# Performance work log

Measured on AMD Instinct MI355X. Metric: run time of the kernel, lower is better.

Reference implementation:

```python
import jax, jax.numpy as jnp
import numpy as np

NMS_THR = 0.5
SCORE_THR = 0.05
MAX_BOXES = 300
N_ANCHORS = 5000
N_CLASSES = 80
IMG = 640.0  # image size used to scale synthetic box coords


def setup_inputs() -> dict:
    key = jax.random.key(0)
    k1, k2, k3 = jax.random.split(key, 3)
    # build well-formed boxes (x1<=x2, y1<=y2) in a 640x640 image
    c1 = jax.random.uniform(k1, (1, N_ANCHORS, 2), jnp.float32) * IMG
    c2 = jax.random.uniform(k2, (1, N_ANCHORS, 2), jnp.float32) * IMG
    boxes = jnp.concatenate([jnp.minimum(c1, c2), jnp.maximum(c1, c2) + 1.0], axis=-1)
    # classification scores in [0,1], squared to skew toward low values like sigmoid logits
    classification = jax.random.uniform(k3, (1, N_ANCHORS, N_CLASSES), jnp.float32) ** 2
    return {"boxes": boxes, "classification": classification}


def _iou_matrix(b):
    # b: [N,4] as (x1,y1,x2,y2) -> [N,N] pairwise IoU
    x1, y1, x2, y2 = b[:, 0], b[:, 1], b[:, 2], b[:, 3]
    area = (x2 - x1) * (y2 - y1)
    iw = jnp.maximum(jnp.minimum(x2[:, None], x2[None, :]) - jnp.maximum(x1[:, None], x1[None, :]), 0.0)
    ih = jnp.maximum(jnp.minimum(y2[:, None], y2[None, :]) - jnp.maximum(y1[:, None], y1[None, :]), 0.0)
    inter = iw * ih
    union = area[:, None] + area[None, :] - inter
    return inter / jnp.maximum(union, 1e-8)


def _nms_one_class(scores, iou):
    # greedy NMS for one class; scores: [N], iou: [N,N] (shared across classes)
    n = scores.shape[0]
    order = jnp.argsort(-scores)          # descending score order
    valid = scores > SCORE_THR            # per-class score-threshold filter
    idxs = jnp.arange(n)

    def step(carry, oi):
        suppressed, kept, count = carry
        alive = (~suppressed[oi]) & valid[oi] & (count < MAX_BOXES)
        # a kept box suppresses all others with IoU above threshold
        suppressed = suppressed | (alive & (iou[oi] > NMS_THR) & (idxs != oi))
        kept = kept.at[oi].set(alive)
        return (suppressed, kept, count + alive.astype(jnp.int32)), None

    init = (jnp.zeros(n, jnp.bool_), jnp.zeros(n, jnp.bool_), jnp.int32(0))
    (_, kept, _), _ = jax.lax.scan(step, init, order)
    return kept  # [N] bool mask in original index space


def reference(boxes, classification):
    b = boxes[0]             # [N,4]
    cls = classification[0]  # [N,C]
    iou = _iou_matrix(b)     # [N,N], class-independent
    kept = jax.vmap(_nms_one_class, in_axes=(1, None))(cls, iou)  # [C,N]
    # scatter surviving scores back to dense per-class score map (zeros elsewhere)
    selected = jnp.where(kept.T, cls, 0.0)                        # [N,C]
    detections = jnp.concatenate([b, selected], axis=1)           # [N,4+C]
    return detections[None]                                       # [1,N,4+C]
```

## Files before the change

### kernel.cpp

```cpp
#include <hip/hip_runtime.h>

#define N_ANCHORS 5000
#define N_CLASSES 80
#define OUT_COLS  84
#define MAX_BOXES 300
#define SCORE_THR 0.05f

#define SORT_PAD  5056
#define NB        4096
#define BLOCK     1024
#define IR        16
#define KR        16
#define DONEP     0x40000000

typedef unsigned long long u64;
typedef unsigned int u32;

#define WG __HIP_MEMORY_SCOPE_WORKGROUP

__device__ __forceinline__ float readlane_f(float v, int l) {
    return __int_as_float(__builtin_amdgcn_readlane(__float_as_int(v), l));
}
__device__ __forceinline__ u32 aload(u32* p) {
    return __hip_atomic_load(p, __ATOMIC_ACQUIRE, WG);
}
__device__ __forceinline__ int bucket_of(float s) {
    float u = sqrtf(s);
    int b = (int)((u - 0.2236f) * 5275.0f);
    return min(max(b, 0), NB - 1);
}
__device__ __forceinline__ bool iou_gt(float4 a, float aa, float4 b, float ab) {
    float iw = fmaxf(fminf(a.z, b.z) - fmaxf(a.x, b.x), 0.0f);
    float ih = fmaxf(fminf(a.w, b.w) - fmaxf(a.y, b.y), 0.0f);
    return 3.0f * (iw * ih) > aa + ab;
}

#define INIT_BLKS 1641
#define TR_BX     157
#define TR_BY     3
#define TR_BLKS   (TR_BX * TR_BY)

__global__ __launch_bounds__(256) void prep(const float* __restrict__ boxes,
                                            const float* __restrict__ cls,
                                            float* __restrict__ clsT,
                                            float* __restrict__ out) {
    __shared__ float tile[32][33];
    int b = blockIdx.x;
    if (b < INIT_BLKS) {
        int i = b * 256 + threadIdx.x;
        if (i < N_ANCHORS * OUT_COLS) {
            int row = i / OUT_COLS, col = i - row * OUT_COLS;
            out[i] = (col < 4) ? boxes[row * 4 + col] : 0.0f;
        }
        return;
    }
    b -= INIT_BLKS;
    int bx_ = b % TR_BX, by_ = b / TR_BX;
    int j0 = bx_ * 32, c0 = by_ * 32;
    int tx = threadIdx.x & 31, ty = threadIdx.x >> 5;
    #pragma unroll
    for (int r = 0; r < 32; r += 8) {
        int j = j0 + ty + r, c = c0 + tx;
        tile[ty + r][tx] = (j < N_ANCHORS && c < N_CLASSES) ? cls[j * N_CLASSES + c] : 0.0f;
    }
    __syncthreads();
    #pragma unroll
    for (int r = 0; r < 32; r += 8) {
        int c = c0 + ty + r, j = j0 + tx;
        if (c < N_CLASSES && j < N_ANCHORS) clsT[(size_t)c * N_ANCHORS + j] = tile[tx][ty + r];
    }
}

__global__ __launch_bounds__(BLOCK, 1) void nms(const float* __restrict__ clsT,
                                                const float4* __restrict__ boxes4,
                                                float* __restrict__ out) {
    __shared__ u64 lk[SORT_PAD];
    __shared__ u32 hist[NB];
    __shared__ float4 kbox[MAX_BOXES + 4];
    __shared__ u64 KS[KR];
    __shared__ u32 flagI[IR], flagK[KR], KBa[KR];
    __shared__ u32 wtot[16];
    __shared__ u32 prog, kcnt;
    u64* Iring = (u64*)hist;

    const int c = blockIdx.x;
    const int t = threadIdx.x;
    const int lane = t & 63;
    const int wv = t >> 6;

    const float4* cp4 = (const float4*)(clsT + (size_t)c * N_ANCHORS);
    u32 sb[8];
    #pragma unroll
    for (int m = 0; m < 2; ++m) {
        int vi = m * 1024 + t;
        float4 v = make_float4(0.f, 0.f, 0.f, 0.f);
        if (vi < N_ANCHORS / 4) v = cp4[vi];
        sb[m * 4 + 0] = (v.x > SCORE_THR) ? __float_as_uint(v.x) : 0u;
        sb[m * 4 + 1] = (v.y > SCORE_THR) ? __float_as_uint(v.y) : 0u;
        sb[m * 4 + 2] = (v.z > SCORE_THR) ? __float_as_uint(v.z) : 0u;
        sb[m * 4 + 3] = (v.w > SCORE_THR) ? __float_as_uint(v.w) : 0u;
    }
    for (int b = t; b < NB; b += BLOCK) hist[b] = 0u;
    if (t < IR) { flagI[t] = 0u; flagK[t] = 0u; }
    if (t == 0) { prog = 0u; kcnt = 0u; }
    __syncthreads();
    #pragma unroll
    for (int m = 0; m < 8; ++m)
        if (sb[m]) atomicAdd(&hist[bucket_of(__uint_as_float(sb[m]))], 1u);
    __syncthreads();

    const int hbase = t * 4;
    u32 vals[4]; u32 run = 0;
    #pragma unroll
    for (int k = 0; k < 4; ++k) { run += hist[hbase + k]; vals[k] = run; }
    u32 x = run;
    #pragma unroll
    for (int off = 1; off < 64; off <<= 1) { u32 y = __shfl_up(x, off); if (lane >= off) x += y; }
    if (lane == 63) wtot[wv] = x;
    __syncthreads();
    u32 woff = 0;
    for (int w = 0; w < wv; ++w) woff += wtot[w];
    const u32 exb = woff + x - run;
    #pragma unroll
    for (int k = 0; k < 4; ++k) hist[hbase + k] = exb + (k ? vals[k - 1] : 0u);
    __syncthreads();
    #pragma unroll
    for (int m = 0; m < 8; ++m) {
        if (sb[m]) {
            int j = ((m >> 2) * 1024 + t) * 4 + (m & 3);
            u32 pos = atomicAdd(&hist[bucket_of(__uint_as_float(sb[m]))], 1u);
            lk[pos] = ((u64)sb[m] << 32) | (u32)(~(u32)j);
        }
    }
    __syncthreads();
    const int total = (int)hist[NB - 1];
    for (int v = total + t; v < SORT_PAD; v += BLOCK) lk[v] = 0ull;
    for (int b = hbase; b < hbase + 4; ++b) {
        int s0 = b ? (int)hist[b - 1] : 0;
        int e  = (int)hist[b];
        for (int i = s0 + 1; i < e; ++i) {
            u64 key = lk[i]; int q = i - 1;
            while (q >= s0 && lk[q] < key) { lk[q + 1] = lk[q]; --q; }
            lk[q + 1] = key;
        }
    }
    __syncthreads();
    const int nch = (total + 63) >> 6;

    if (wv >= 1 && wv <= 8) {
        for (int j = wv - 1; j < nch; j += 8) {
            u32 p;
            for (;;) {
                p = aload(&prog);
                if ((int)p >= j - (IR - 1)) break;
                __builtin_amdgcn_s_sleep(2);
            }
            if (p >= DONEP) return;
            u64 e = lk[j * 64 + lane];
            u32 jj = e ? ~(u32)e : 0u;
            float4 bx = boxes4[jj];
            float ar = (bx.z - bx.x) * (bx.w - bx.y);
            u64 word = 0ull;
            #pragma unroll 16
            for (int q = 0; q < 64; ++q) {
                float4 o;
                o.x = readlane_f(bx.x, q); o.y = readlane_f(bx.y, q);
                o.z = readlane_f(bx.z, q); o.w = readlane_f(bx.w, q);
                float ao = (o.z - o.x) * (o.w - o.y);
                if (iou_gt(bx, ar, o, ao)) word |= (1ull << q);
            }
            Iring[(j & (IR - 1)) * 64 + lane] = word;
            if (lane == 0)
                __hip_atomic_store(&flagI[j & (IR - 1)], (u32)(j + 1), __ATOMIC_RELEASE, WG);
        }
        return;
    }
    if (wv >= 9) {
        for (int j = wv - 9; j < nch; j += 7) {
            u32 p;
            for (;;) {
                p = aload(&prog);
                if ((int)p >= j - 6) break;
                __builtin_amdgcn_s_sleep(2);
            }
            if (p >= DONEP) return;
            u64 e = lk[j * 64 + lane];
            u32 jj = e ? ~(u32)e : 0u;
            float4 bx = boxes4[jj];
            float ar = (bx.z - bx.x) * (bx.w - bx.y);
            u32 ka = aload(&kcnt);
            bool sup = false;
            for (u32 r = 0; r < ka; ++r) {
                float4 q = kbox[r];
                float aq = (q.z - q.x) * (q.w - q.y);
                if (iou_gt(bx, ar, q, aq)) sup = true;
            }
            for (;;) {
                p = aload(&prog);
                if ((int)p >= j - 2) break;
                __builtin_amdgcn_s_sleep(2);
            }
            u32 kb2 = (p >= DONEP) ? ka : aload(&kcnt);
            for (u32 r = ka; r < kb2; ++r) {
                float4 q = kbox[r];
                float aq = (q.z - q.x) * (q.w - q.y);
                if (iou_gt(bx, ar, q, aq)) sup = true;
            }
            u64 ksw = __ballot(sup);
            if (lane == 0) {
                KS[j & (KR - 1)] = ksw;
                KBa[j & (KR - 1)] = kb2;
                __hip_atomic_store(&flagK[j & (KR - 1)], (u32)(j + 1), __ATOMIC_RELEASE, WG);
            }
            if (p >= DONEP) return;
        }
        return;
    }

    int kept = 0; u32 kcur = 0; bool capped = false;
    for (int k = 0; k < nch; ++k) {
        u64 key = lk[k * 64 + lane];
        bool valid = (key != 0ull);
        u32 j = valid ? ~(u32)key : 0u;
        float sc = __uint_as_float((u32)(key >> 32));
        float4 bx = boxes4[j];
        float ar = (bx.z - bx.x) * (bx.w - bx.y);

        while (aload(&flagK[k & (KR - 1)]) != (u32)(k + 1)) __builtin_amdgcn_s_sleep(1);
        u64 ks = KS[k & (KR - 1)];
        u32 kb = KBa[k & (KR - 1)];
        bool alive = valid && !((ks >> lane) & 1ull);
        for (u32 r = kb; r < kcur; ++r) {
            float4 q = kbox[r];
            float aq = (q.z - q.x) * (q.w - q.y);
            if (iou_gt(bx, ar, q, aq)) alive = false;
        }

        while (aload(&flagI[k & (IR - 1)]) != (u32)(k + 1)) __builtin_amdgcn_s_sleep(1);
        u64 I = Iring[(k & (IR - 1)) * 64 + lane];

        u64 rem = __ballot(alive);
        u64 km = 0ull;
        while (rem) {
            int pos = __ffsll((long long)rem) - 1;
            km |= 1ull << pos;
            if (++kept == MAX_BOXES) { capped = true; break; }
            u32 lo = (u32)__builtin_amdgcn_readlane((int)(u32)I, pos);
            u32 hi = (u32)__builtin_amdgcn_readlane((int)(u32)(I >> 32), pos);
            rem &= ~(((u64)hi << 32) | (u64)lo);
        }
        int nk = __popcll(km);
        if ((km >> lane) & 1ull) {
            out[(size_t)j * OUT_COLS + 4 + c] = sc;
            kbox[kcur + __popcll(km & ((1ull << lane) - 1ull))] = bx;
        }
        kcur += (u32)nk;
        if (capped) break;
        if (lane == 0) {
            __hip_atomic_store(&kcnt, kcur, __ATOMIC_RELAXED, WG);
            __hip_atomic_store(&prog, (u32)(k + 1), __ATOMIC_RELEASE, WG);
        }
    }
    if (lane == 0) __hip_atomic_store(&prog, (u32)DONEP, __ATOMIC_RELEASE, WG);
}

extern "C" void kernel_launch(void* const* d_in, const int* in_sizes, int n_in,
                              void* d_out, int out_size, void* d_ws, size_t ws_size,
                              hipStream_t stream) {
    const float* boxes = (const float*)d_in[0];
    const float* cls   = (const float*)d_in[1];
    float* out = (float*)d_out;
    float* clsT = (float*)d_ws;

    prep<<<INIT_BLKS + TR_BLKS, 256, 0, stream>>>(boxes, cls, clsT, out);
    nms<<<N_CLASSES, BLOCK, 0, stream>>>(clsT, (const float4*)boxes, out);
}
```

Measured before the change: 140.6 us.

## Rebalance NMS wave roles and skip intra-chunk IoU for pre-suppressed boxes

Reassigns waves so only two compute intra-chunk IoU words and thirteen run the kept-box suppression check. The suppression waves publish an early mask, which the IoU waves use to skip columns already suppressed. The suppression loops exit early once every lane is suppressed. The serial leader wave prefetches the next chunk's key and box, busy-spins instead of sleeping, and skips fully suppressed chunks without waiting for the IoU word. This adds handshake complexity and risks stalls from the reduced IoU wave count.

```diff
diff --git a/kernel.cpp b/kernel.cpp
--- a/kernel.cpp
+++ b/kernel.cpp
@@ -9,8 +9,7 @@
 #define SORT_PAD  5056
 #define NB        4096
 #define BLOCK     1024
-#define IR        16
-#define KR        16
+#define SLOTS     16
 #define DONEP     0x40000000
 
 typedef unsigned long long u64;
@@ -76,9 +75,9 @@
                                                 float* __restrict__ out) {
     __shared__ u64 lk[SORT_PAD];
     __shared__ u32 hist[NB];
-    __shared__ float4 kbox[MAX_BOXES + 4];
-    __shared__ u64 KS[KR];
-    __shared__ u32 flagI[IR], flagK[KR], KBa[KR];
+    __shared__ float4 kbox[MAX_BOXES + 8];
+    __shared__ u64 KS[SLOTS], KSA[SLOTS];
+    __shared__ u32 flagI[SLOTS], flagK[SLOTS], flagKA[SLOTS], KBa[SLOTS];
     __shared__ u32 wtot[16];
     __shared__ u32 prog, kcnt;
     u64* Iring = (u64*)hist;
@@ -101,7 +100,7 @@
         sb[m * 4 + 3] = (v.w > SCORE_THR) ? __float_as_uint(v.w) : 0u;
     }
     for (int b = t; b < NB; b += BLOCK) hist[b] = 0u;
-    if (t < IR) { flagI[t] = 0u; flagK[t] = 0u; }
+    if (t < SLOTS) { flagI[t] = 0u; flagK[t] = 0u; flagKA[t] = 0u; }
     if (t == 0) { prog = 0u; kcnt = 0u; }
     __syncthreads();
     #pragma unroll
@@ -147,70 +146,90 @@
     __syncthreads();
     const int nch = (total + 63) >> 6;
 
-    if (wv >= 1 && wv <= 8) {
-        for (int j = wv - 1; j < nch; j += 8) {
+    if (wv == 1 || wv == 2) {
+        for (int j = wv - 1; j < nch; j += 2) {
+            const int slot = j & (SLOTS - 1);
             u32 p;
             for (;;) {
                 p = aload(&prog);
-                if ((int)p >= j - (IR - 1)) break;
-                __builtin_amdgcn_s_sleep(2);
+                if ((int)p >= j - 8) break;
+                __builtin_amdgcn_s_sleep(4);
             }
             if (p >= DONEP) return;
             u64 e = lk[j * 64 + lane];
             u32 jj = e ? ~(u32)e : 0u;
             float4 bx = boxes4[jj];
             float ar = (bx.z - bx.x) * (bx.w - bx.y);
-            u64 word = 0ull;
-            #pragma unroll 16
-            for (int q = 0; q < 64; ++q) {
+            for (;;) {
+                u32 f = aload(&flagKA[slot]);
+                if (f == (u32)(j + 1)) break;
+                if (aload(&prog) >= DONEP) return;
+                __builtin_amdgcn_s_sleep(1);
+            }
+            u64 S = ~KSA[slot];
+            u64 word = 0ull, mset = S;
+            while (mset) {
+                int q = __ffsll((long long)mset) - 1;
+                mset &= mset - 1;
                 float4 o;
                 o.x = readlane_f(bx.x, q); o.y = readlane_f(bx.y, q);
                 o.z = readlane_f(bx.z, q); o.w = readlane_f(bx.w, q);
                 float ao = (o.z - o.x) * (o.w - o.y);
                 if (iou_gt(bx, ar, o, ao)) word |= (1ull << q);
             }
-            Iring[(j & (IR - 1)) * 64 + lane] = word;
+            Iring[slot * 64 + lane] = word;
             if (lane == 0)
-                __hip_atomic_store(&flagI[j & (IR - 1)], (u32)(j + 1), __ATOMIC_RELEASE, WG);
+                __hip_atomic_store(&flagI[slot], (u32)(j + 1), __ATOMIC_RELEASE, WG);
         }
         return;
     }
-    if (wv >= 9) {
-        for (int j = wv - 9; j < nch; j += 7) {
+    if (wv >= 3) {
+        for (int j = wv - 3; j < nch; j += 13) {
+            const int slot = j & (SLOTS - 1);
             u32 p;
             for (;;) {
                 p = aload(&prog);
-                if ((int)p >= j - 6) break;
-                __builtin_amdgcn_s_sleep(2);
+                if ((int)p >= j - 10) break;
+                __builtin_amdgcn_s_sleep(4);
             }
             if (p >= DONEP) return;
             u64 e = lk[j * 64 + lane];
-            u32 jj = e ? ~(u32)e : 0u;
+            bool validL = (e != 0ull);
+            u32 jj = validL ? ~(u32)e : 0u;
             float4 bx = boxes4[jj];
             float ar = (bx.z - bx.x) * (bx.w - bx.y);
+            bool sup = !validL;
             u32 ka = aload(&kcnt);
-            bool sup = false;
-            for (u32 r = 0; r < ka; ++r) {
+            u64 livem = __ballot(!sup);
+            for (u32 r = 0; r < ka && livem; ++r) {
                 float4 q = kbox[r];
                 float aq = (q.z - q.x) * (q.w - q.y);
-                if (iou_gt(bx, ar, q, aq)) sup = true;
+                if (!sup && iou_gt(bx, ar, q, aq)) sup = true;
+                if ((r & 7u) == 7u) livem = __ballot(!sup);
+            }
+            u64 ksa = __ballot(sup);
+            if (lane == 0) {
+                KSA[slot] = ksa;
+                __hip_atomic_store(&flagKA[slot], (u32)(j + 1), __ATOMIC_RELEASE, WG);
             }
             for (;;) {
                 p = aload(&prog);
                 if ((int)p >= j - 2) break;
-                __builtin_amdgcn_s_sleep(2);
+                __builtin_amdgcn_s_sleep(1);
             }
             u32 kb2 = (p >= DONEP) ? ka : aload(&kcnt);
-            for (u32 r = ka; r < kb2; ++r) {
+            if (kb2 < ka) kb2 = ka;
+            u64 livem2 = __ballot(!sup);
+            for (u32 r = ka; r < kb2 && livem2; ++r) {
                 float4 q = kbox[r];
                 float aq = (q.z - q.x) * (q.w - q.y);
-                if (iou_gt(bx, ar, q, aq)) sup = true;
-            }
-            u64 ksw = __ballot(sup);
+                if (!sup && iou_gt(bx, ar, q, aq)) sup = true;
+                if ((r & 7u) == 7u) livem2 = __ballot(!sup);
+            }
+            u64 ks = __ballot(sup);
             if (lane == 0) {
-                KS[j & (KR - 1)] = ksw;
-                KBa[j & (KR - 1)] = kb2;
-                __hip_atomic_store(&flagK[j & (KR - 1)], (u32)(j + 1), __ATOMIC_RELEASE, WG);
+                KS[slot] = ks; KBa[slot] = kb2;
+                __hip_atomic_store(&flagK[slot], (u32)(j + 1), __ATOMIC_RELEASE, WG);
             }
             if (p >= DONEP) return;
         }
@@ -218,48 +237,56 @@
     }
 
     int kept = 0; u32 kcur = 0; bool capped = false;
+    u64 key = (nch > 0) ? lk[lane] : 0ull;
+    float4 bx = boxes4[key ? ~(u32)key : 0u];
     for (int k = 0; k < nch; ++k) {
-        u64 key = lk[k * 64 + lane];
+        const int slot = k & (SLOTS - 1);
+        u64 keyN = 0ull; float4 bxN = bx;
+        if (k + 1 < nch) {
+            keyN = lk[(k + 1) * 64 + lane];
+            bxN = boxes4[keyN ? ~(u32)keyN : 0u];
+        }
         bool valid = (key != 0ull);
         u32 j = valid ? ~(u32)key : 0u;
         float sc = __uint_as_float((u32)(key >> 32));
-        float4 bx = boxes4[j];
-        float ar = (bx.z - bx.x) * (bx.w - bx.y);
-
-        while (aload(&flagK[k & (KR - 1)]) != (u32)(k + 1)) __builtin_amdgcn_s_sleep(1);
-        u64 ks = KS[k & (KR - 1)];
-        u32 kb = KBa[k & (KR - 1)];
-        bool alive = valid && !((ks >> lane) & 1ull);
-        for (u32 r = kb; r < kcur; ++r) {
-            float4 q = kbox[r];
-            float aq = (q.z - q.x) * (q.w - q.y);
-            if (iou_gt(bx, ar, q, aq)) alive = false;
-        }
-
-        while (aload(&flagI[k & (IR - 1)]) != (u32)(k + 1)) __builtin_amdgcn_s_sleep(1);
-        u64 I = Iring[(k & (IR - 1)) * 64 + lane];
-
-        u64 rem = __ballot(alive);
-        u64 km = 0ull;
-        while (rem) {
-            int pos = __ffsll((long long)rem) - 1;
-            km |= 1ull << pos;
-            if (++kept == MAX_BOXES) { capped = true; break; }
-            u32 lo = (u32)__builtin_amdgcn_readlane((int)(u32)I, pos);
-            u32 hi = (u32)__builtin_amdgcn_readlane((int)(u32)(I >> 32), pos);
-            rem &= ~(((u64)hi << 32) | (u64)lo);
-        }
-        int nk = __popcll(km);
-        if ((km >> lane) & 1ull) {
-            out[(size_t)j * OUT_COLS + 4 + c] = sc;
-            kbox[kcur + __popcll(km & ((1ull << lane) - 1ull))] = bx;
-        }
-        kcur += (u32)nk;
+
+        while (aload(&flagK[slot]) != (u32)(k + 1)) { }
+        u64 ks = KS[slot];
+        if (ks != ~0ull) {
+            u32 kb = KBa[slot];
+            float ar = (bx.z - bx.x) * (bx.w - bx.y);
+            bool alive = valid && !((ks >> lane) & 1ull);
+            for (u32 r = kb; r < kcur; ++r) {
+                float4 q = kbox[r];
+                float aq = (q.z - q.x) * (q.w - q.y);
+                if (alive && iou_gt(bx, ar, q, aq)) alive = false;
+            }
+            u64 rem = __ballot(alive);
+            if (rem) {
+                while (aload(&flagI[slot]) != (u32)(k + 1)) { }
+                u64 I = Iring[slot * 64 + lane];
+                u64 km = 0ull;
+                while (rem) {
+                    int pos = __ffsll((long long)rem) - 1;
+                    km |= 1ull << pos;
+                    if (++kept == MAX_BOXES) { capped = true; break; }
+                    u32 lo = (u32)__builtin_amdgcn_readlane((int)(u32)I, pos);
+                    u32 hi = (u32)__builtin_amdgcn_readlane((int)(u32)(I >> 32), pos);
+                    rem &= ~(((u64)hi << 32) | (u64)lo);
+                }
+                if ((km >> lane) & 1ull) {
+                    out[(size_t)j * OUT_COLS + 4 + c] = sc;
+                    kbox[kcur + __popcll(km & ((1ull << lane) - 1ull))] = bx;
+                }
+                kcur += (u32)__popcll(km);
+            }
+        }
         if (capped) break;
         if (lane == 0) {
             __hip_atomic_store(&kcnt, kcur, __ATOMIC_RELAXED, WG);
             __hip_atomic_store(&prog, (u32)(k + 1), __ATOMIC_RELEASE, WG);
         }
+        key = keyN; bx = bxN;
     }
     if (lane == 0) __hip_atomic_store(&prog, (u32)DONEP, __ATOMIC_RELEASE, WG);
 }
```

Result: slower. 211.9 us (+50.6%).
